# Performance work log

Hardware: AMD Instinct MI355X
Metric: run time of the kernel (lower is better)

Reference implementation:

```python
import jax, jax.numpy as jnp
import numpy as np

EMBD_SIZE = 128
NUM_HEADS = 8
HEAD_SIZE = 16

def setup_inputs() -> dict:
    key = jax.random.key(0)
    ks = jax.random.split(key, 6)
    B, S = 8, 2048
    x = jax.random.normal(ks[0], (B, S, EMBD_SIZE), dtype=jnp.float32)
    # per-head Linear weights, torch layout [out, in] stacked over heads -> [H, hs, E]
    sc = 1.0 / np.sqrt(EMBD_SIZE)
    Wk = jax.random.normal(ks[1], (NUM_HEADS, HEAD_SIZE, EMBD_SIZE), dtype=jnp.float32) * sc
    Wq = jax.random.normal(ks[2], (NUM_HEADS, HEAD_SIZE, EMBD_SIZE), dtype=jnp.float32) * sc
    Wv = jax.random.normal(ks[3], (NUM_HEADS, HEAD_SIZE, EMBD_SIZE), dtype=jnp.float32) * sc
    Wp = jax.random.normal(ks[4], (EMBD_SIZE, NUM_HEADS * HEAD_SIZE), dtype=jnp.float32) * sc
    bp = jax.random.normal(ks[5], (EMBD_SIZE,), dtype=jnp.float32) * 0.01
    return {"x": x, "Wk": Wk, "Wq": Wq, "Wv": Wv, "Wp": Wp, "bp": bp}

def reference(x, Wk, Wq, Wv, Wp, bp):
    # x: [B,S,E]; W{k,q,v}: [H,hs,E]; Wp: [E,H*hs]
    B, S, E = x.shape
    H, hs, _ = Wk.shape
    q = jnp.einsum('bse,hde->bhsd', x, Wq)
    k = jnp.einsum('bse,hde->bhsd', x, Wk)
    v = jnp.einsum('bse,hde->bhsd', x, Wv)
    # NOTE: original code MULTIPLIES by sqrt(head_size) (k.shape[-1]**0.5)
    scores = jnp.einsum('bhsd,bhtd->bhst', q, k) * (hs ** 0.5)
    wei = jax.nn.softmax(scores, axis=-1)  # dropout is identity in eval mode
    out = jnp.einsum('bhst,bhtd->bhsd', wei, v)
    # concat heads along last dim: [B,S,H*hs]
    out = out.transpose(0, 2, 1, 3).reshape(B, S, H * hs)
    return out @ Wp.T + bp
```

## Files before the change

kernel.cpp:

```cpp
#include <hip/hip_runtime.h>
#include <hip/hip_bf16.h>

constexpr int Bb  = 8;
constexpr int Ss  = 2048;
constexpr int Ee  = 128;
constexpr int Hh  = 8;
constexpr int HSs = 16;
constexpr int QKVSZ = Bb * Hh * Ss * HSs;

typedef _Float16 f16;
typedef __attribute__((ext_vector_type(8)))  _Float16 f16x8;
typedef __attribute__((ext_vector_type(16))) float f32x16;

constexpr float QSCALE = 5.770780163555854f;

__device__ __forceinline__ unsigned pack_rtz(float lo, float hi) {
    union { __fp16 __attribute__((ext_vector_type(2))) h; unsigned u; } c;
    c.h = __builtin_amdgcn_cvt_pkrtz(lo, hi);
    return c.u;
}
__device__ __forceinline__ unsigned pack_rne(float lo, float hi) {
    union { __attribute__((ext_vector_type(2))) _Float16 h; unsigned u; } c;
    c.h[0] = (f16)lo; c.h[1] = (f16)hi;
    return c.u;
}

__device__ __forceinline__ float vmax16(const f32x16& v) {
    float a = fmaxf(fmaxf(v[0],  v[1]),  v[2]);
    float b = fmaxf(fmaxf(v[3],  v[4]),  v[5]);
    float c = fmaxf(fmaxf(v[6],  v[7]),  v[8]);
    float d = fmaxf(fmaxf(v[9],  v[10]), v[11]);
    float e = fmaxf(fmaxf(v[12], v[13]), v[14]);
    float g = fmaxf(fmaxf(a, b), c);
    float h = fmaxf(fmaxf(d, e), v[15]);
    return fmaxf(g, h);
}

__device__ __forceinline__ f16x8 cvt8(const float4& w0, const float4& w1) {
    union { f16x8 v; unsigned u[4]; } wf;
    wf.u[0] = pack_rne(w0.x, w0.y); wf.u[1] = pack_rne(w0.z, w0.w);
    wf.u[2] = pack_rne(w1.x, w1.y); wf.u[3] = pack_rne(w1.z, w1.w);
    return wf.v;
}

__global__ __launch_bounds__(512, 4) void qkv_kernel(
    const float* __restrict__ x,
    const float* __restrict__ Wq, const float* __restrict__ Wk,
    const float* __restrict__ Wv,
    f16* __restrict__ qo, f16* __restrict__ ko, f16* __restrict__ vo)
{
    constexpr int LDW = 136;
    __shared__ __align__(16) f16 Xs[32 * LDW];

    const int rowbase = blockIdx.x * 32;

    for (int idx = threadIdx.x; idx < 32 * 32; idx += 512) {
        const int r = idx >> 5, cp = idx & 31;
        float4 v = *(const float4*)(x + (size_t)(rowbase + r) * Ee + cp * 4);
        union { f16 h[4]; uint2 u; } cv;
        cv.h[0] = (f16)v.x; cv.h[1] = (f16)v.y; cv.h[2] = (f16)v.z; cv.h[3] = (f16)v.w;
        *(uint2*)&Xs[r * LDW + cp * 4] = cv.u;
    }
    __syncthreads();

    const int wid = threadIdx.x >> 6, lane = threadIdx.x & 63;
    const int h = lane >> 5, n31 = lane & 31;

    f16x8 Xf[8];
#pragma unroll
    for (int t = 0; t < 8; ++t)
        Xf[t] = *(const f16x8*)&Xs[n31 * LDW + 16 * t + 8 * h];

    const int b = rowbase >> 11;
    const int s0 = rowbase & 2047;

    if (wid < 4) {
        const int s = s0 + n31;
#pragma unroll
        for (int mat = 0; mat < 2; ++mat) {
            const float* W = (mat == 0) ? Wq : Wk;
            const float* wr32 = W + (size_t)(wid * 32 + n31) * Ee + 8 * h;
            f32x16 acc = {};
#pragma unroll
            for (int t = 0; t < 8; ++t) {
                float4 w0 = *(const float4*)(wr32 + 16 * t);
                float4 w1 = *(const float4*)(wr32 + 16 * t + 4);
                acc = __builtin_amdgcn_mfma_f32_32x32x16_f16(cvt8(w0, w1), Xf[t], acc, 0, 0, 0);
            }
            f16* dst = (mat == 0) ? qo : ko;
            const float scale = (mat == 1) ? QSCALE : 1.f;
#pragma unroll
            for (int rq = 0; rq < 4; ++rq) {
                const int cbase = wid * 32 + 8 * rq + 4 * h;
                const int head = cbase >> 4, dbase = cbase & 15;
                union { f16 hv[4]; uint2 u; } pk4;
#pragma unroll
                for (int i = 0; i < 4; ++i) pk4.hv[i] = (f16)(acc[4 * rq + i] * scale);
                *(uint2*)(dst + ((size_t)(b * Hh + head) * Ss + s) * HSs + dbase) = pk4.u;
            }
        }
    } else {
        const int g = wid - 4;
        const int c = g * 32 + n31;
        const int head = c >> 4, d = c & 15;
        const int bh = b * Hh + head;
        const int it = s0 >> 6, g0 = (s0 >> 4) & 3;
        const float* wr32 = Wv + (size_t)c * Ee + 8 * h;
        f32x16 acc = {};
#pragma unroll
        for (int t = 0; t < 8; ++t) {
            float4 w0 = *(const float4*)(wr32 + 16 * t);
            float4 w1 = *(const float4*)(wr32 + 16 * t + 4);
            acc = __builtin_amdgcn_mfma_f32_32x32x16_f16(Xf[t], cvt8(w0, w1), acc, 0, 0, 0);
        }
        f16* vb = vo + (size_t)bh * 65536 + it * 2048;
#pragma unroll
        for (int rq = 0; rq < 4; ++rq) {
            union { f16 hv[4]; uint2 u; } pk4;
#pragma unroll
            for (int i = 0; i < 4; ++i) pk4.hv[i] = (f16)acc[4 * rq + i];
            *(uint2*)(vb + (g0 + (rq >> 1)) * 512 + (d + 32 * h) * 8 + 4 * (rq & 1)) = pk4.u;
        }

        for (int i = threadIdx.x - 256; i < 512; i += 256) {
            const int gp = i >> 8, hd = (i >> 5) & 7, cc = i & 31;
            const int lanep = (cc < 16) ? 16 + cc : 32 + cc;
            const unsigned one2 = 0x3C003C00u;
            uint4 val = ((cc & 15) == 0) ? (uint4){one2, one2, one2, one2}
                                         : (uint4){0, 0, 0, 0};
            *(uint4*)(vo + (size_t)(b * Hh + hd) * 65536 + it * 2048
                      + (g0 + gp) * 512 + lanep * 8) = val;
        }
    }
}

__global__ __launch_bounds__(512, 4) void attn_kernel(
    const f16* __restrict__ qg, const f16* __restrict__ kg,
    const f16* __restrict__ vg, const float* __restrict__ wp32,
    const float* __restrict__ bp, float* __restrict__ out)
{
    constexpr int LDW = 136;
    __shared__ __align__(16) f16 Os[32 * LDW];

    const int b    = blockIdx.x & 7;
    const int qblk = blockIdx.x >> 3;
    const int wid  = threadIdx.x >> 6;
    const int lane = threadIdx.x & 63;
    const int h    = lane >> 5;
    const int q31  = lane & 31;
    const int qbase = qblk * 32;
    const int bh   = b * Hh + wid;

    const f16x8 qf = *(const f16x8*)(qg + ((size_t)bh * Ss + qbase + q31) * HSs + 8 * h);

    const f16* pk = kg + (size_t)bh * Ss * HSs + q31 * 16 + 8 * h;
    const f16* pv = vg + (size_t)bh * 65536 + lane * 8;

    f16x8 ka0 = *(const f16x8*)pk;
    f16x8 ka1 = *(const f16x8*)(pk + 512);
    f16x8 va0 = *(const f16x8*)(pv);
    f16x8 va1 = *(const f16x8*)(pv + 512);
    f16x8 va2 = *(const f16x8*)(pv + 1024);
    f16x8 va3 = *(const f16x8*)(pv + 1536);

    f32x16 acc = {};
    f32x16 cinit = {};

    constexpr int NIT = Ss / 64;
    for (int it = 0; it < NIT; ++it) {
        f32x16 st0 = __builtin_amdgcn_mfma_f32_32x32x16_f16(ka0, qf, cinit, 0, 0, 0);
        f32x16 st1 = __builtin_amdgcn_mfma_f32_32x32x16_f16(ka1, qf, cinit, 0, 0, 0);

        if (it + 1 < NIT) {
            pk += 1024;
            ka0 = *(const f16x8*)pk;
            ka1 = *(const f16x8*)(pk + 512);
        }

        float mx = fmaxf(vmax16(st0), vmax16(st1));
        mx = fmaxf(mx, __shfl_xor(mx, 32, 64));

        if (__any(mx > 8.f)) {
            const float delta = fmaxf(mx, 0.f);
            const float corr  = __builtin_amdgcn_exp2f(-delta);
#pragma unroll
            for (int r = 0; r < 9; ++r) acc[r] *= corr;
#pragma unroll
            for (int t = 0; t < 16; ++t) { st0[t] -= delta; st1[t] -= delta; }
#pragma unroll
            for (int r = 0; r < 16; ++r) cinit[r] -= delta;
        }

        union { unsigned u[4]; f16x8 v; } B1, B2, B3, B4;
#pragma unroll
        for (int r = 0; r < 4; ++r) {
            B1.u[r] = pack_rtz(__builtin_amdgcn_exp2f(st0[2 * r]),
                               __builtin_amdgcn_exp2f(st0[2 * r + 1]));
            B2.u[r] = pack_rtz(__builtin_amdgcn_exp2f(st0[8 + 2 * r]),
                               __builtin_amdgcn_exp2f(st0[9 + 2 * r]));
            B3.u[r] = pack_rtz(__builtin_amdgcn_exp2f(st1[2 * r]),
                               __builtin_amdgcn_exp2f(st1[2 * r + 1]));
            B4.u[r] = pack_rtz(__builtin_amdgcn_exp2f(st1[8 + 2 * r]),
                               __builtin_amdgcn_exp2f(st1[9 + 2 * r]));
        }

        __builtin_amdgcn_s_setprio(1);
        acc = __builtin_amdgcn_mfma_f32_32x32x16_f16(va0, B1.v, acc, 0, 0, 0);
        acc = __builtin_amdgcn_mfma_f32_32x32x16_f16(va1, B2.v, acc, 0, 0, 0);
        acc = __builtin_amdgcn_mfma_f32_32x32x16_f16(va2, B3.v, acc, 0, 0, 0);
        acc = __builtin_amdgcn_mfma_f32_32x32x16_f16(va3, B4.v, acc, 0, 0, 0);
        __builtin_amdgcn_s_setprio(0);

        if (it + 1 < NIT) {
            pv += 2048;
            va0 = *(const f16x8*)(pv);
            va1 = *(const f16x8*)(pv + 512);
            va2 = *(const f16x8*)(pv + 1024);
            va3 = *(const f16x8*)(pv + 1536);
        }
    }

    const float l = acc[8] + __shfl_xor(acc[8], 32, 64);
    const float inv = 1.f / l;

    f16* orow = &Os[q31 * LDW + wid * HSs + 4 * h];
    uint2 lo = { pack_rne(acc[0] * inv, acc[1] * inv), pack_rne(acc[2] * inv, acc[3] * inv) };
    uint2 hi = { pack_rne(acc[4] * inv, acc[5] * inv), pack_rne(acc[6] * inv, acc[7] * inv) };
    *(uint2*)(orow)     = lo;
    *(uint2*)(orow + 8) = hi;
    __syncthreads();

    if (wid >= 4) return;

    f16x8 A[8];
#pragma unroll
    for (int t = 0; t < 8; ++t)
        A[t] = *(const f16x8*)&Os[q31 * LDW + 16 * t + 8 * h];

    const int e = wid * 32 + q31;
    const float* wr32 = wp32 + (size_t)e * Ee + 8 * h;
    f32x16 acc2 = {};
#pragma unroll
    for (int t = 0; t < 8; ++t) {
        float4 w0 = *(const float4*)(wr32 + 16 * t);
        float4 w1 = *(const float4*)(wr32 + 16 * t + 4);
        acc2 = __builtin_amdgcn_mfma_f32_32x32x16_f16(A[t], cvt8(w0, w1), acc2, 0, 0, 0);
    }

    const float bias = bp[e];
#pragma unroll
    for (int r = 0; r < 16; ++r) {
        const int R = qbase + (r & 3) + 8 * (r >> 2) + 4 * h;
        out[((size_t)b * Ss + R) * Ee + e] = acc2[r] + bias;
    }
}

extern "C" void kernel_launch(void* const* d_in, const int* in_sizes, int n_in,
                              void* d_out, int out_size, void* d_ws, size_t ws_size,
                              hipStream_t stream)
{
    const float* x  = (const float*)d_in[0];
    const float* Wk = (const float*)d_in[1];
    const float* Wq = (const float*)d_in[2];
    const float* Wv = (const float*)d_in[3];
    const float* Wp = (const float*)d_in[4];
    const float* bp = (const float*)d_in[5];
    float* out = (float*)d_out;

    f16* ws = (f16*)d_ws;
    f16* qh = ws;
    f16* kh = ws + (size_t)QKVSZ;
    f16* vh = ws + (size_t)2 * QKVSZ;

    qkv_kernel<<<Bb * Ss / 32, 512, 0, stream>>>(x, Wq, Wk, Wv, qh, kh, vh);
    attn_kernel<<<Bb * Ss / 32, 512, 0, stream>>>(qh, kh, vh, Wp, bp, out);
}
```

Baseline: 132.9 us.

## Split attention over key halves with separate merge and projection kernel

The attention kernel is split into a first pass that handles half the key sequence per block, using 256-thread blocks covering four heads, which quadruples the block count. Partial normalized outputs plus per-row max and sum are written to workspace. A second kernel merges the two halves with log-sum-exp weights and then applies the output projection. The PV accumulation is also split into two independent accumulators to shorten the MFMA dependency chain. In exchange it adds an extra launch and a round trip of partial results through global memory.

```diff
diff --git a/kernel.cpp b/kernel.cpp
--- a/kernel.cpp
+++ b/kernel.cpp
@@ -134,27 +134,27 @@
     }
 }
 
-__global__ __launch_bounds__(512, 4) void attn_kernel(
+__global__ __launch_bounds__(256, 4) void attn_pass1(
     const f16* __restrict__ qg, const f16* __restrict__ kg,
-    const f16* __restrict__ vg, const float* __restrict__ wp32,
-    const float* __restrict__ bp, float* __restrict__ out)
+    const f16* __restrict__ vg, f16* __restrict__ po, float* __restrict__ pml)
 {
-    constexpr int LDW = 136;
-    __shared__ __align__(16) f16 Os[32 * LDW];
-
-    const int b    = blockIdx.x & 7;
-    const int qblk = blockIdx.x >> 3;
+    const int blk  = blockIdx.x;
+    const int b    = blk & 7;
+    const int qt   = (blk >> 3) & 63;
+    const int hg   = (blk >> 9) & 1;
+    const int half = (blk >> 10) & 1;
     const int wid  = threadIdx.x >> 6;
     const int lane = threadIdx.x & 63;
     const int h    = lane >> 5;
     const int q31  = lane & 31;
-    const int qbase = qblk * 32;
-    const int bh   = b * Hh + wid;
+    const int head = hg * 4 + wid;
+    const int bh   = b * Hh + head;
+    const int qbase = qt * 32;
 
     const f16x8 qf = *(const f16x8*)(qg + ((size_t)bh * Ss + qbase + q31) * HSs + 8 * h);
 
-    const f16* pk = kg + (size_t)bh * Ss * HSs + q31 * 16 + 8 * h;
-    const f16* pv = vg + (size_t)bh * 65536 + lane * 8;
+    const f16* pk = kg + (size_t)bh * Ss * HSs + half * 16384 + q31 * 16 + 8 * h;
+    const f16* pv = vg + (size_t)bh * 65536 + half * 32768 + lane * 8;
 
     f16x8 ka0 = *(const f16x8*)pk;
     f16x8 ka1 = *(const f16x8*)(pk + 512);
@@ -163,10 +163,11 @@
     f16x8 va2 = *(const f16x8*)(pv + 1024);
     f16x8 va3 = *(const f16x8*)(pv + 1536);
 
-    f32x16 acc = {};
+    f32x16 accA = {};
+    f32x16 accB = {};
     f32x16 cinit = {};
 
-    constexpr int NIT = Ss / 64;
+    constexpr int NIT = (Ss / 2) / 64;
     for (int it = 0; it < NIT; ++it) {
         f32x16 st0 = __builtin_amdgcn_mfma_f32_32x32x16_f16(ka0, qf, cinit, 0, 0, 0);
         f32x16 st1 = __builtin_amdgcn_mfma_f32_32x32x16_f16(ka1, qf, cinit, 0, 0, 0);
@@ -184,7 +185,7 @@
             const float delta = fmaxf(mx, 0.f);
             const float corr  = __builtin_amdgcn_exp2f(-delta);
 #pragma unroll
-            for (int r = 0; r < 9; ++r) acc[r] *= corr;
+            for (int r = 0; r < 9; ++r) { accA[r] *= corr; accB[r] *= corr; }
 #pragma unroll
             for (int t = 0; t < 16; ++t) { st0[t] -= delta; st1[t] -= delta; }
 #pragma unroll
@@ -205,10 +206,10 @@
         }
 
         __builtin_amdgcn_s_setprio(1);
-        acc = __builtin_amdgcn_mfma_f32_32x32x16_f16(va0, B1.v, acc, 0, 0, 0);
-        acc = __builtin_amdgcn_mfma_f32_32x32x16_f16(va1, B2.v, acc, 0, 0, 0);
-        acc = __builtin_amdgcn_mfma_f32_32x32x16_f16(va2, B3.v, acc, 0, 0, 0);
-        acc = __builtin_amdgcn_mfma_f32_32x32x16_f16(va3, B4.v, acc, 0, 0, 0);
+        accA = __builtin_amdgcn_mfma_f32_32x32x16_f16(va0, B1.v, accA, 0, 0, 0);
+        accB = __builtin_amdgcn_mfma_f32_32x32x16_f16(va1, B2.v, accB, 0, 0, 0);
+        accA = __builtin_amdgcn_mfma_f32_32x32x16_f16(va2, B3.v, accA, 0, 0, 0);
+        accB = __builtin_amdgcn_mfma_f32_32x32x16_f16(va3, B4.v, accB, 0, 0, 0);
         __builtin_amdgcn_s_setprio(0);
 
         if (it + 1 < NIT) {
@@ -220,14 +221,65 @@
         }
     }
 
-    const float l = acc[8] + __shfl_xor(acc[8], 32, 64);
+    float l = accA[8] + accB[8];
+    l += __shfl_xor(l, 32, 64);
     const float inv = 1.f / l;
-
-    f16* orow = &Os[q31 * LDW + wid * HSs + 4 * h];
-    uint2 lo = { pack_rne(acc[0] * inv, acc[1] * inv), pack_rne(acc[2] * inv, acc[3] * inv) };
-    uint2 hi = { pack_rne(acc[4] * inv, acc[5] * inv), pack_rne(acc[6] * inv, acc[7] * inv) };
+    const float m = -cinit[0];
+
+    f16* pb = po + ((((size_t)half * 64 + bh) * 64 + qt) * 32 + q31) * 16;
+    uint2 w0 = { pack_rne((accA[0] + accB[0]) * inv, (accA[1] + accB[1]) * inv),
+                 pack_rne((accA[2] + accB[2]) * inv, (accA[3] + accB[3]) * inv) };
+    uint2 w1 = { pack_rne((accA[4] + accB[4]) * inv, (accA[5] + accB[5]) * inv),
+                 pack_rne((accA[6] + accB[6]) * inv, (accA[7] + accB[7]) * inv) };
+    *(uint2*)(pb + 4 * h)     = w0;
+    *(uint2*)(pb + 8 + 4 * h) = w1;
+
+    if (h == 0) {
+        float2 ml = { m, l };
+        *(float2*)(pml + ((((size_t)half * 64 + bh) * 64 + qt) * 32 + q31) * 2) = ml;
+    }
+}
+
+__global__ __launch_bounds__(512, 4) void merge_proj(
+    const f16* __restrict__ po, const float* __restrict__ pml,
+    const float* __restrict__ wp32, const float* __restrict__ bp,
+    float* __restrict__ out)
+{
+    constexpr int LDW = 136;
+    __shared__ __align__(16) f16 Os[32 * LDW];
+    constexpr size_t HALF_O  = (size_t)64 * 64 * 32 * 16;
+    constexpr size_t HALF_ML = (size_t)64 * 64 * 32 * 2;
+
+    const int b    = blockIdx.x & 7;
+    const int qt   = blockIdx.x >> 3;
+    const int qbase = qt * 32;
+    const int wid  = threadIdx.x >> 6;
+    const int lane = threadIdx.x & 63;
+    const int h    = lane >> 5;
+    const int q31  = lane & 31;
+    const int bh   = b * Hh + wid;
+
+    const size_t ob = (((size_t)bh * 64 + qt) * 32 + q31) * 16 + 8 * h;
+    f16x8 o1 = *(const f16x8*)(po + ob);
+    f16x8 o2 = *(const f16x8*)(po + HALF_O + ob);
+    const size_t mb = (((size_t)bh * 64 + qt) * 32 + q31) * 2;
+    float2 ml1 = *(const float2*)(pml + mb);
+    float2 ml2 = *(const float2*)(pml + HALF_ML + mb);
+
+    const float M  = fmaxf(ml1.x, ml2.x);
+    float w1 = ml1.y * __builtin_amdgcn_exp2f(ml1.x - M);
+    float w2 = ml2.y * __builtin_amdgcn_exp2f(ml2.x - M);
+    const float winv = 1.f / (w1 + w2);
+    w1 *= winv; w2 *= winv;
+
+    float om[8];
+#pragma unroll
+    for (int j = 0; j < 8; ++j) om[j] = (float)o1[j] * w1 + (float)o2[j] * w2;
+    uint2 lo = { pack_rne(om[0], om[1]), pack_rne(om[2], om[3]) };
+    uint2 hi = { pack_rne(om[4], om[5]), pack_rne(om[6], om[7]) };
+    f16* orow = &Os[q31 * LDW + wid * HSs + 8 * h];
     *(uint2*)(orow)     = lo;
-    *(uint2*)(orow + 8) = hi;
+    *(uint2*)(orow + 4) = hi;
     __syncthreads();
 
     if (wid >= 4) return;
@@ -243,8 +295,8 @@
 #pragma unroll
     for (int t = 0; t < 8; ++t) {
         float4 w0 = *(const float4*)(wr32 + 16 * t);
-        float4 w1 = *(const float4*)(wr32 + 16 * t + 4);
-        acc2 = __builtin_amdgcn_mfma_f32_32x32x16_f16(A[t], cvt8(w0, w1), acc2, 0, 0, 0);
+        float4 w1v = *(const float4*)(wr32 + 16 * t + 4);
+        acc2 = __builtin_amdgcn_mfma_f32_32x32x16_f16(A[t], cvt8(w0, w1v), acc2, 0, 0, 0);
     }
 
     const float bias = bp[e];
@@ -271,7 +323,10 @@
     f16* qh = ws;
     f16* kh = ws + (size_t)QKVSZ;
     f16* vh = ws + (size_t)2 * QKVSZ;
+    f16* po = ws + (size_t)4 * QKVSZ;
+    float* pml = (float*)(ws + (size_t)6 * QKVSZ);
 
     qkv_kernel<<<Bb * Ss / 32, 512, 0, stream>>>(x, Wq, Wk, Wv, qh, kh, vh);
-    attn_kernel<<<Bb * Ss / 32, 512, 0, stream>>>(qh, kh, vh, Wp, bp, out);
-}
+    attn_pass1<<<2 * 2 * 64 * 8, 256, 0, stream>>>(qh, kh, vh, po, pml);
+    merge_proj<<<Bb * Ss / 32, 512, 0, stream>>>(po, pml, Wp, bp, out);
+}
```

New measurement: 139.5 us. 1.05x slower.
